# Kernel tuning notes

Measured on AMD Instinct MI355X. Metric: run time of the kernel, lower is better.

## Reference

```python
import jax, jax.numpy as jnp
import numpy as np


def setup_inputs() -> dict:
    key = jax.random.key(0)
    ks = jax.random.split(key, 8)
    N, E, IN, ED, P, OUT = 50000, 400000, 128, 16, 3, 128
    return {
        "x": jax.random.normal(ks[0], (N, IN), dtype=jnp.float32),
        "edge_index": jax.random.randint(ks[1], (2, E), 0, N, dtype=jnp.int64),
        "edge_attr": jax.random.normal(ks[2], (E, ED), dtype=jnp.float32),
        "edge_time": jax.random.uniform(ks[3], (E,), dtype=jnp.float32),
        "current_time": jnp.ones((), dtype=jnp.float32),
        "W": jax.random.normal(ks[4], (P, IN + ED, OUT), dtype=jnp.float32) / np.sqrt(IN + ED),
        "b": jax.random.normal(ks[5], (P, OUT), dtype=jnp.float32) * 0.01,
        "decay": jnp.ones((P,), dtype=jnp.float32),
    }


def reference(x, edge_index, edge_attr, edge_time, current_time, W, b, decay):
    # x: [N, in_dim]; edge_index: [2, E]; edge_attr: [E, edge_dim]
    N = x.shape[0]
    src, dst = edge_index[0], edge_index[1]
    combined = jnp.concatenate([x[src], edge_attr], axis=-1)        # [E, in+edge]
    messages = jnp.einsum('ef,pfo->epo', combined, W) + b[None]     # [E, P, out]
    time_delta = current_time - edge_time                           # [E]
    temporal_weight = jnp.exp(-decay[None, :] * time_delta[:, None])  # [E, P]
    weighted = messages * temporal_weight[:, :, None]               # [E, P, out]
    # scatter-add per destination node -> [N, P, out]
    return jax.ops.segment_sum(weighted, dst, num_segments=N)
```

## Files before the change

### kernel.cpp

```cpp
#include <hip/hip_runtime.h>
#include <stdint.h>

#define N_NODES 50000
#define E_EDGES 400000
#define IN_DIM  128
#define ED_DIM  16
#define K_DIM   144
#define KT_N    5
#define P_N     3
#define OUT_DIM 128
#define NCOL    384
#define NT_N    24
#define ETILE   64
#define NBLK    6250
#define ASTRIDE 168

#define NC_PAD  50176
#define SCAN_T  1024
#define SCAN_C  49

typedef float  f32x4  __attribute__((ext_vector_type(4)));
typedef __bf16 bf16x8 __attribute__((ext_vector_type(8)));

__device__ __forceinline__ unsigned short f2bf(float f) {
    union { float f; unsigned u; } v; v.f = f;
    unsigned u = v.u + 0x7fffu + ((v.u >> 16) & 1u);
    return (unsigned short)(u >> 16);
}

__global__ void pack_w(const float* __restrict__ W, unsigned short* __restrict__ Bpack) {
    int idx = blockIdx.x * blockDim.x + threadIdx.x;
    if (idx >= NT_N * KT_N * 64 * 8) return;
    int j    = idx & 7;
    int lane = (idx >> 3) & 63;
    int kt   = (idx >> 9) % KT_N;
    int nt   = idx / (KT_N * 512);
    int nc   = lane & 15;
    int kr   = ((lane >> 4) << 3) + j;
    int f    = kt * 32 + kr;
    int n    = nt * 16 + nc;
    int p    = n >> 7;
    int o    = n & 127;
    float val = (f < K_DIM) ? W[(p * K_DIM + f) * OUT_DIM + o] : 0.0f;
    Bpack[idx] = f2bf(val);
}

__global__ void k_hist(const int* __restrict__ ei, int* __restrict__ counts) {
    int e = blockIdx.x * 256 + threadIdx.x;
    if (e < E_EDGES) atomicAdd(&counts[ei[E_EDGES + e]], 1);
}

__global__ __launch_bounds__(SCAN_T) void k_scan(const int* __restrict__ counts,
                                                 int* __restrict__ cursor) {
    __shared__ int tsum[SCAN_T];
    const int t = threadIdx.x;
    const int base = t * SCAN_C;
    int s = 0;
    for (int i = 0; i < SCAN_C; ++i) s += counts[base + i];
    tsum[t] = s;
    __syncthreads();
    for (int off = 1; off < SCAN_T; off <<= 1) {
        int add = (t >= off) ? tsum[t - off] : 0;
        __syncthreads();
        tsum[t] += add;
        __syncthreads();
    }
    int run = tsum[t] - s;
    for (int i = 0; i < SCAN_C; ++i) {
        int c = counts[base + i];
        cursor[base + i] = run;
        run += c;
    }
}

__global__ void k_scatter(const int* __restrict__ ei, const float* __restrict__ etime,
                          int* __restrict__ cursor, int4* __restrict__ equad) {
    int e = blockIdx.x * 256 + threadIdx.x;
    if (e >= E_EDGES) return;
    int d = ei[E_EDGES + e];
    int pos = atomicAdd(&cursor[d], 1);
    int4 q;
    q.x = ei[e];
    q.y = e;
    q.z = d;
    q.w = __float_as_int(etime[e]);
    equad[pos] = q;
}

__global__ __launch_bounds__(512) void mpc_phaseB(
    const float* __restrict__ x,
    const float* __restrict__ edge_attr,
    const float* __restrict__ current_time,
    const unsigned short* __restrict__ Bpack,
    const float* __restrict__ bvec,
    const float* __restrict__ decay,
    const int4*  __restrict__ equad,
    float* __restrict__ out)
{
    __shared__ __align__(16) unsigned short Alds[ETILE][ASTRIDE];
    __shared__ int   src_lds[ETILE];
    __shared__ int   pe_lds[ETILE];
    __shared__ int   dst_lds[ETILE];
    __shared__ float wt_lds[ETILE][P_N];
    __shared__ int   pn_dst[2];

    const int tid = threadIdx.x;
    const int e0  = blockIdx.x * ETILE;
    const float ct = current_time[0];

    if (tid < ETILE) {
        int4 q = equad[e0 + tid];
        src_lds[tid] = q.x;
        pe_lds[tid]  = q.y;
        dst_lds[tid] = q.z;
        float dtv = ct - __int_as_float(q.w);
        wt_lds[tid][0] = __expf(-decay[0] * dtv);
        wt_lds[tid][1] = __expf(-decay[1] * dtv);
        wt_lds[tid][2] = __expf(-decay[2] * dtv);
    } else if (tid == ETILE) {
        const int* ez = (const int*)equad;
        pn_dst[0] = (e0 > 0) ? ez[(size_t)(e0 - 1) * 4 + 2] : -1;
        pn_dst[1] = (e0 + ETILE < E_EDGES) ? ez[(size_t)(e0 + ETILE) * 4 + 2] : -1;
    }
    __syncthreads();

    const float4* x4  = (const float4*)x;
    const float4* ea4 = (const float4*)edge_attr;
    for (int i = tid; i < ETILE * 40; i += 512) {
        int e = i / 40, q = i % 40;
        int se = (((e >> 2) & 3) << 4) | (((e >> 4) & 3) << 2) | (e & 3);
        uint2 val;
        if (q < 36) {
            float4 v;
            if (q < 32) v = x4[(size_t)src_lds[se] * 32 + q];
            else        v = ea4[(size_t)pe_lds[se] * 4 + (q - 32)];
            unsigned lo = (unsigned)f2bf(v.x) | ((unsigned)f2bf(v.y) << 16);
            unsigned hi = (unsigned)f2bf(v.z) | ((unsigned)f2bf(v.w) << 16);
            val = make_uint2(lo, hi);
        } else {
            val = make_uint2(0u, 0u);
        }
        *(uint2*)&Alds[e][q * 4] = val;
    }
    __syncthreads();

    const int w    = tid >> 6;
    const int lane = tid & 63;
    const int row  = lane & 15;
    const int khi  = lane >> 4;

    f32x4 acc[4][3];
#pragma unroll
    for (int mi = 0; mi < 4; ++mi)
#pragma unroll
        for (int ni = 0; ni < 3; ++ni)
            acc[mi][ni] = (f32x4){0.f, 0.f, 0.f, 0.f};

#pragma unroll
    for (int kt = 0; kt < KT_N; ++kt) {
        bf16x8 a[4], bf[3];
#pragma unroll
        for (int mi = 0; mi < 4; ++mi)
            a[mi] = *(const bf16x8*)&Alds[mi * 16 + row][kt * 32 + khi * 8];
#pragma unroll
        for (int ni = 0; ni < 3; ++ni) {
            int nt = w * 3 + ni;
            bf[ni] = *(const bf16x8*)&Bpack[(size_t)(((nt * KT_N) + kt) * 64 + lane) * 8];
        }
#pragma unroll
        for (int mi = 0; mi < 4; ++mi)
#pragma unroll
            for (int ni = 0; ni < 3; ++ni)
                acc[mi][ni] = __builtin_amdgcn_mfma_f32_16x16x32_bf16(
                    a[mi], bf[ni], acc[mi][ni], 0, 0, 0);
    }

    int   ncol[3], pcol[3];
    float bval[3];
#pragma unroll
    for (int ni = 0; ni < 3; ++ni) {
        ncol[ni] = (w * 3 + ni) * 16 + row;
        pcol[ni] = ncol[ni] >> 7;
        bval[ni] = bvec[ncol[ni]];
    }

    const int sbase = khi * 16;
    int dsp[16];
#pragma unroll
    for (int t = 0; t < 16; ++t) dsp[t] = dst_lds[sbase + t];
    const int prev_dst = (khi > 0) ? dst_lds[sbase - 1]  : pn_dst[0];
    const int next_dst = (khi < 3) ? dst_lds[sbase + 16] : pn_dst[1];

#pragma unroll
    for (int ni = 0; ni < 3; ++ni) {
        const int n = ncol[ni], p = pcol[ni];
        const float bv = bval[ni];
        float run = 0.0f;
        int   rd  = dsp[0];
        bool  head = true;
#pragma unroll
        for (int t = 0; t < 16; ++t) {
            float c = (acc[t >> 2][ni][t & 3] + bv) * wt_lds[sbase + t][p];
            int d = dsp[t];
            if (d != rd) {
                float* dst = &out[(size_t)rd * NCOL + n];
                if (head && rd == prev_dst) atomicAdd(dst, run);
                else                        *dst = run;
                head = false;
                run = 0.0f;
                rd  = d;
            }
            run += c;
        }
        float* dst = &out[(size_t)rd * NCOL + n];
        if ((head && rd == prev_dst) || rd == next_dst) atomicAdd(dst, run);
        else                                            *dst = run;
    }
}

extern "C" void kernel_launch(void* const* d_in, const int* in_sizes, int n_in,
                              void* d_out, int out_size, void* d_ws, size_t ws_size,
                              hipStream_t stream) {
    const float* x            = (const float*)d_in[0];
    const int*   edge_index   = (const int*)d_in[1];
    const float* edge_attr    = (const float*)d_in[2];
    const float* edge_time    = (const float*)d_in[3];
    const float* current_time = (const float*)d_in[4];
    const float* W            = (const float*)d_in[5];
    const float* bvec         = (const float*)d_in[6];
    const float* decay        = (const float*)d_in[7];
    float* out = (float*)d_out;

    char* ws = (char*)d_ws;
    unsigned short* Bpack = (unsigned short*)(ws);
    int*   counts  = (int*)  (ws + 122880);
    int*   cursor  = (int*)  (ws + 323584);
    int4*  equad   = (int4*) (ws + 524288);

    hipMemsetAsync(counts, 0, (size_t)NC_PAD * 4, stream);
    hipMemsetAsync(d_out, 0, (size_t)out_size * sizeof(float), stream);

    pack_w<<<(NT_N * KT_N * 64 * 8 + 255) / 256, 256, 0, stream>>>(W, Bpack);

    k_hist   <<<(E_EDGES + 255) / 256, 256, 0, stream>>>(edge_index, counts);
    k_scan   <<<1, SCAN_T, 0, stream>>>(counts, cursor);
    k_scatter<<<(E_EDGES + 255) / 256, 256, 0, stream>>>(edge_index, edge_time, cursor, equad);

    mpc_phaseB<<<NBLK, 512, 0, stream>>>(x, edge_attr, current_time, Bpack, bvec,
                                         decay, equad, out);
}
```

Baseline: 342.5 us.

## Double-buffer edge tiles per block to overlap gather with MFMA and scatter

Each block now processes four 64-edge tiles in a loop with double-buffered LDS, prefetching the next tile's metadata and x/edge_attr rows while computing and scattering the current tile. The goal is to hide global gather latency behind the MFMA and scatter phases and to amortise the B-fragment/bias setup. It also swaps the manual float-to-bf16 rounding for the packed v_cvt_pk_bf16_f32 instruction. The trade-offs are doubled LDS footprint, more registers held across the loop, and a smaller grid, all of which can reduce occupancy and load balance.

```diff
diff --git a/kernel.cpp b/kernel.cpp
--- a/kernel.cpp
+++ b/kernel.cpp
@@ -12,7 +12,9 @@
 #define NCOL    384
 #define NT_N    24
 #define ETILE   64
-#define NBLK    6250
+#define NTILES  6250
+#define TPB     4
+#define NBLK9   1563
 #define ASTRIDE 168
 
 #define NC_PAD  50176
@@ -26,6 +28,12 @@
     union { float f; unsigned u; } v; v.f = f;
     unsigned u = v.u + 0x7fffu + ((v.u >> 16) & 1u);
     return (unsigned short)(u >> 16);
+}
+
+__device__ __forceinline__ unsigned cvt_pk_bf16(float a, float b) {
+    unsigned r;
+    asm("v_cvt_pk_bf16_f32 %0, %1, %2" : "=v"(r) : "v"(a), "v"(b));
+    return r;
 }
 
 __global__ void pack_w(const float* __restrict__ W, unsigned short* __restrict__ Bpack) {
@@ -97,84 +105,27 @@
     const int4*  __restrict__ equad,
     float* __restrict__ out)
 {
-    __shared__ __align__(16) unsigned short Alds[ETILE][ASTRIDE];
-    __shared__ int   src_lds[ETILE];
-    __shared__ int   pe_lds[ETILE];
-    __shared__ int   dst_lds[ETILE];
-    __shared__ float wt_lds[ETILE][P_N];
-    __shared__ int   pn_dst[2];
+    __shared__ __align__(16) unsigned short Alds[2][ETILE][ASTRIDE];
+    __shared__ int   src_lds[2][ETILE];
+    __shared__ int   pe_lds [2][ETILE];
+    __shared__ int   dst_lds[2][ETILE];
+    __shared__ float wt_lds [2][ETILE][P_N];
+    __shared__ int   pn_lds [2][2];
 
     const int tid = threadIdx.x;
-    const int e0  = blockIdx.x * ETILE;
+    const int t0  = blockIdx.x * TPB;
+    const int nt_blk = min(TPB, NTILES - t0);
     const float ct = current_time[0];
-
-    if (tid < ETILE) {
-        int4 q = equad[e0 + tid];
-        src_lds[tid] = q.x;
-        pe_lds[tid]  = q.y;
-        dst_lds[tid] = q.z;
-        float dtv = ct - __int_as_float(q.w);
-        wt_lds[tid][0] = __expf(-decay[0] * dtv);
-        wt_lds[tid][1] = __expf(-decay[1] * dtv);
-        wt_lds[tid][2] = __expf(-decay[2] * dtv);
-    } else if (tid == ETILE) {
-        const int* ez = (const int*)equad;
-        pn_dst[0] = (e0 > 0) ? ez[(size_t)(e0 - 1) * 4 + 2] : -1;
-        pn_dst[1] = (e0 + ETILE < E_EDGES) ? ez[(size_t)(e0 + ETILE) * 4 + 2] : -1;
-    }
-    __syncthreads();
 
     const float4* x4  = (const float4*)x;
     const float4* ea4 = (const float4*)edge_attr;
-    for (int i = tid; i < ETILE * 40; i += 512) {
-        int e = i / 40, q = i % 40;
-        int se = (((e >> 2) & 3) << 4) | (((e >> 4) & 3) << 2) | (e & 3);
-        uint2 val;
-        if (q < 36) {
-            float4 v;
-            if (q < 32) v = x4[(size_t)src_lds[se] * 32 + q];
-            else        v = ea4[(size_t)pe_lds[se] * 4 + (q - 32)];
-            unsigned lo = (unsigned)f2bf(v.x) | ((unsigned)f2bf(v.y) << 16);
-            unsigned hi = (unsigned)f2bf(v.z) | ((unsigned)f2bf(v.w) << 16);
-            val = make_uint2(lo, hi);
-        } else {
-            val = make_uint2(0u, 0u);
-        }
-        *(uint2*)&Alds[e][q * 4] = val;
-    }
-    __syncthreads();
+    const int*    ez  = (const int*)equad;
 
     const int w    = tid >> 6;
     const int lane = tid & 63;
     const int row  = lane & 15;
     const int khi  = lane >> 4;
 
-    f32x4 acc[4][3];
-#pragma unroll
-    for (int mi = 0; mi < 4; ++mi)
-#pragma unroll
-        for (int ni = 0; ni < 3; ++ni)
-            acc[mi][ni] = (f32x4){0.f, 0.f, 0.f, 0.f};
-
-#pragma unroll
-    for (int kt = 0; kt < KT_N; ++kt) {
-        bf16x8 a[4], bf[3];
-#pragma unroll
-        for (int mi = 0; mi < 4; ++mi)
-            a[mi] = *(const bf16x8*)&Alds[mi * 16 + row][kt * 32 + khi * 8];
-#pragma unroll
-        for (int ni = 0; ni < 3; ++ni) {
-            int nt = w * 3 + ni;
-            bf[ni] = *(const bf16x8*)&Bpack[(size_t)(((nt * KT_N) + kt) * 64 + lane) * 8];
-        }
-#pragma unroll
-        for (int mi = 0; mi < 4; ++mi)
-#pragma unroll
-            for (int ni = 0; ni < 3; ++ni)
-                acc[mi][ni] = __builtin_amdgcn_mfma_f32_16x16x32_bf16(
-                    a[mi], bf[ni], acc[mi][ni], 0, 0, 0);
-    }
-
     int   ncol[3], pcol[3];
     float bval[3];
 #pragma unroll
@@ -184,37 +135,154 @@
         bval[ni] = bvec[ncol[ni]];
     }
 
-    const int sbase = khi * 16;
-    int dsp[16];
-#pragma unroll
-    for (int t = 0; t < 16; ++t) dsp[t] = dst_lds[sbase + t];
-    const int prev_dst = (khi > 0) ? dst_lds[sbase - 1]  : pn_dst[0];
-    const int next_dst = (khi < 3) ? dst_lds[sbase + 16] : pn_dst[1];
-
-#pragma unroll
-    for (int ni = 0; ni < 3; ++ni) {
-        const int n = ncol[ni], p = pcol[ni];
-        const float bv = bval[ni];
-        float run = 0.0f;
-        int   rd  = dsp[0];
-        bool  head = true;
-#pragma unroll
-        for (int t = 0; t < 16; ++t) {
-            float c = (acc[t >> 2][ni][t & 3] + bv) * wt_lds[sbase + t][p];
-            int d = dsp[t];
-            if (d != rd) {
+    int ce[5], cq[5], cse[5];
+#pragma unroll
+    for (int u = 0; u < 5; ++u) {
+        int i = tid + u * 512;
+        ce[u] = i / 40;
+        cq[u] = i % 40;
+        int e = ce[u];
+        cse[u] = (((e >> 2) & 3) << 4) | (((e >> 4) & 3) << 2) | (e & 3);
+    }
+
+    {
+        int e0 = t0 * ETILE;
+        if (tid < ETILE) {
+            int4 q = equad[e0 + tid];
+            src_lds[0][tid] = q.x;
+            pe_lds [0][tid] = q.y;
+            dst_lds[0][tid] = q.z;
+            float dtv = ct - __int_as_float(q.w);
+            wt_lds[0][tid][0] = __expf(-decay[0] * dtv);
+            wt_lds[0][tid][1] = __expf(-decay[1] * dtv);
+            wt_lds[0][tid][2] = __expf(-decay[2] * dtv);
+        } else if (tid == ETILE) {
+            pn_lds[0][0] = (e0 > 0) ? ez[(size_t)(e0 - 1) * 4 + 2] : -1;
+            pn_lds[0][1] = (e0 + ETILE < E_EDGES) ? ez[(size_t)(e0 + ETILE) * 4 + 2] : -1;
+        }
+        __syncthreads();
+#pragma unroll
+        for (int u = 0; u < 5; ++u) {
+            uint2 val;
+            if (cq[u] < 36) {
+                float4 v;
+                if (cq[u] < 32) v = x4[(size_t)src_lds[0][cse[u]] * 32 + cq[u]];
+                else            v = ea4[(size_t)pe_lds[0][cse[u]] * 4 + (cq[u] - 32)];
+                val = make_uint2(cvt_pk_bf16(v.x, v.y), cvt_pk_bf16(v.z, v.w));
+            } else val = make_uint2(0u, 0u);
+            *(uint2*)&Alds[0][ce[u]][cq[u] * 4] = val;
+        }
+    }
+
+    for (int k = 0; k < nt_blk; ++k) {
+        const int cur = k & 1, nxt = cur ^ 1;
+        const bool pf = (k + 1 < nt_blk);
+        __syncthreads();
+
+        int4 mq; int mp0 = -1, mp1 = -1;
+        if (pf) {
+            int e0n = (t0 + k + 1) * ETILE;
+            if (tid < ETILE) mq = equad[e0n + tid];
+            else if (tid == ETILE) {
+                mp0 = ez[(size_t)(e0n - 1) * 4 + 2];
+                mp1 = (e0n + ETILE < E_EDGES) ? ez[(size_t)(e0n + ETILE) * 4 + 2] : -1;
+            }
+        }
+
+        f32x4 acc[4][3];
+#pragma unroll
+        for (int mi = 0; mi < 4; ++mi)
+#pragma unroll
+            for (int ni = 0; ni < 3; ++ni)
+                acc[mi][ni] = (f32x4){0.f, 0.f, 0.f, 0.f};
+#pragma unroll
+        for (int kt = 0; kt < KT_N; ++kt) {
+            bf16x8 a[4], bf[3];
+#pragma unroll
+            for (int mi = 0; mi < 4; ++mi)
+                a[mi] = *(const bf16x8*)&Alds[cur][mi * 16 + row][kt * 32 + khi * 8];
+#pragma unroll
+            for (int ni = 0; ni < 3; ++ni) {
+                int nt = w * 3 + ni;
+                bf[ni] = *(const bf16x8*)&Bpack[(size_t)(((nt * KT_N) + kt) * 64 + lane) * 8];
+            }
+#pragma unroll
+            for (int mi = 0; mi < 4; ++mi)
+#pragma unroll
+                for (int ni = 0; ni < 3; ++ni)
+                    acc[mi][ni] = __builtin_amdgcn_mfma_f32_16x16x32_bf16(
+                        a[mi], bf[ni], acc[mi][ni], 0, 0, 0);
+        }
+
+        if (pf) {
+            if (tid < ETILE) {
+                src_lds[nxt][tid] = mq.x;
+                pe_lds [nxt][tid] = mq.y;
+                dst_lds[nxt][tid] = mq.z;
+                float dtv = ct - __int_as_float(mq.w);
+                wt_lds[nxt][tid][0] = __expf(-decay[0] * dtv);
+                wt_lds[nxt][tid][1] = __expf(-decay[1] * dtv);
+                wt_lds[nxt][tid][2] = __expf(-decay[2] * dtv);
+            } else if (tid == ETILE) {
+                pn_lds[nxt][0] = mp0;
+                pn_lds[nxt][1] = mp1;
+            }
+        }
+        __syncthreads();
+
+        float4 g[5];
+        if (pf) {
+#pragma unroll
+            for (int u = 0; u < 5; ++u) {
+                if (cq[u] < 32)      g[u] = x4[(size_t)src_lds[nxt][cse[u]] * 32 + cq[u]];
+                else if (cq[u] < 36) g[u] = ea4[(size_t)pe_lds[nxt][cse[u]] * 4 + (cq[u] - 32)];
+            }
+        }
+
+        {
+            const int sbase = khi * 16;
+            int dsp[16];
+#pragma unroll
+            for (int t = 0; t < 16; ++t) dsp[t] = dst_lds[cur][sbase + t];
+            const int prev_dst = (khi > 0) ? dst_lds[cur][sbase - 1]  : pn_lds[cur][0];
+            const int next_dst = (khi < 3) ? dst_lds[cur][sbase + 16] : pn_lds[cur][1];
+#pragma unroll
+            for (int ni = 0; ni < 3; ++ni) {
+                const int n = ncol[ni], p = pcol[ni];
+                const float bv = bval[ni];
+                float run = 0.0f;
+                int   rd  = dsp[0];
+                bool  head = true;
+#pragma unroll
+                for (int t = 0; t < 16; ++t) {
+                    float c = (acc[t >> 2][ni][t & 3] + bv) * wt_lds[cur][sbase + t][p];
+                    int d = dsp[t];
+                    if (d != rd) {
+                        float* dst = &out[(size_t)rd * NCOL + n];
+                        if (head && rd == prev_dst) atomicAdd(dst, run);
+                        else                        *dst = run;
+                        head = false;
+                        run = 0.0f;
+                        rd  = d;
+                    }
+                    run += c;
+                }
                 float* dst = &out[(size_t)rd * NCOL + n];
-                if (head && rd == prev_dst) atomicAdd(dst, run);
-                else                        *dst = run;
-                head = false;
-                run = 0.0f;
-                rd  = d;
-            }
-            run += c;
-        }
-        float* dst = &out[(size_t)rd * NCOL + n];
-        if ((head && rd == prev_dst) || rd == next_dst) atomicAdd(dst, run);
-        else                                            *dst = run;
+                if ((head && rd == prev_dst) || rd == next_dst) atomicAdd(dst, run);
+                else                                            *dst = run;
+            }
+        }
+
+        if (pf) {
+#pragma unroll
+            for (int u = 0; u < 5; ++u) {
+                uint2 val;
+                if (cq[u] < 36)
+                    val = make_uint2(cvt_pk_bf16(g[u].x, g[u].y), cvt_pk_bf16(g[u].z, g[u].w));
+                else val = make_uint2(0u, 0u);
+                *(uint2*)&Alds[nxt][ce[u]][cq[u] * 4] = val;
+            }
+        }
     }
 }
 
@@ -246,6 +314,6 @@
     k_scan   <<<1, SCAN_T, 0, stream>>>(counts, cursor);
     k_scatter<<<(E_EDGES + 255) / 256, 256, 0, stream>>>(edge_index, edge_time, cursor, equad);
 
-    mpc_phaseB<<<NBLK, 512, 0, stream>>>(x, edge_attr, current_time, Bpack, bvec,
-                                         decay, equad, out);
-}
+    mpc_phaseB<<<NBLK9, 512, 0, stream>>>(x, edge_attr, current_time, Bpack, bvec,
+                                          decay, equad, out);
+}
```

New measurement: 393.2 us. 1.15x slower.
